# Kernel tuning notes

Hardware: AMD Instinct MI355X
Metric: run time of the kernel (lower is better)

## Reference

```python
import jax, jax.numpy as jnp
import numpy as np
from jax import lax

N, CIN, COUT, T, V = 32, 64, 128, 256, 25
IC = COUT // 4
EPS = 1e-5


def setup_inputs() -> dict:
    key = jax.random.key(0)
    ks = jax.random.split(key, 16)
    rn = lambda k, shape, s=0.05: jax.random.normal(k, shape, jnp.float32) * s
    inp = {
        'x': jax.random.normal(ks[0], (N, CIN, T, V), jnp.float32),
        'A': rn(ks[1], (V, V), 0.2),
        'w1': rn(ks[2], (IC, CIN)), 'b1': rn(ks[3], (IC,), 0.01),
        'w2': rn(ks[4], (IC, CIN)), 'b2': rn(ks[5], (IC,), 0.01),
        'w3': rn(ks[6], (COUT, CIN)), 'b3': rn(ks[7], (COUT,), 0.01),
        'w4': rn(ks[8], (COUT, CIN)), 'b4': rn(ks[9], (COUT,), 0.01),
        'bn1_g': jnp.ones((COUT,)), 'bn1_b': jnp.zeros((COUT,)),
        'bn1_m': rn(ks[10], (COUT,), 0.1), 'bn1_v': jnp.ones((COUT,)),
        'wt': rn(ks[11], (COUT, COUT, 9, 1)), 'bt': rn(ks[12], (COUT,), 0.01),
        'bn2_g': jnp.ones((COUT,)), 'bn2_b': jnp.zeros((COUT,)),
        'bn2_m': rn(ks[13], (COUT,), 0.1), 'bn2_v': jnp.ones((COUT,)),
        'wr': rn(ks[14], (COUT, CIN)), 'br': rn(ks[15], (COUT,), 0.01),
        'bnr_g': jnp.ones((COUT,)), 'bnr_b': jnp.zeros((COUT,)),
        'bnr_m': jnp.zeros((COUT,)), 'bnr_v': jnp.ones((COUT,)),
    }
    return inp


def _conv1x1(x, w, b):
    # 1x1 Conv2d over (T,V): pure channel mix. x: [N,C,T,V], w: [O,C]
    return jnp.einsum('oc,nctv->notv', w, x) + b[None, :, None, None]


def _bn(x, g, b, m, v):
    # BatchNorm2d in eval mode (running stats)
    scale = g / jnp.sqrt(v + EPS)
    return x * scale[None, :, None, None] + (b - m * scale)[None, :, None, None]


def _forward(x, A, w1, b1, w2, b2, w3, b3, w4, b4,
             bn1_g, bn1_b, bn1_m, bn1_v, wt, bt,
             bn2_g, bn2_b, bn2_m, bn2_v, wr, br,
             bnr_g, bnr_b, bnr_m, bnr_v):
    n, _, t, v = x.shape
    cout = w3.shape[0]
    ic = cout // 4
    x1 = _conv1x1(x, w1, b1).mean(axis=2)  # [N,IC,V]
    x2 = _conv1x1(x, w2, b2).mean(axis=2)  # [N,IC,V]
    a = jax.nn.softmax(x1[..., :, None] - x2[..., None, :], axis=-1)  # [N,IC,V,V]
    x3 = _conv1x1(x, w3, b3).reshape(n, 4, ic, t, v)
    y = jnp.einsum('ncuv,nmctv->nmctu', a, x3).reshape(n, cout, t, v)
    y = y + jnp.einsum('uv,nctv->nctu', A, _conv1x1(x, w4, b4))
    # tcn: BN -> ReLU -> Conv2d (9,1) pad (4,0) -> BN
    y = jax.nn.relu(_bn(y, bn1_g, bn1_b, bn1_m, bn1_v))
    y = lax.conv_general_dilated(
        y, wt, window_strides=(1, 1), padding=[(4, 4), (0, 0)],
        dimension_numbers=('NCHW', 'OIHW', 'NCHW')) + bt[None, :, None, None]
    y = _bn(y, bn2_g, bn2_b, bn2_m, bn2_v)
    # residual branch (in_channels != out_channels): 1x1 conv + BN
    res = _bn(_conv1x1(x, wr, br), bnr_g, bnr_b, bnr_m, bnr_v)
    return jax.nn.relu(y + res)


def reference(x, A, w1, b1, w2, b2, w3, b3, w4, b4,
              bn1_g, bn1_b, bn1_m, bn1_v, wt, bt,
              bn2_g, bn2_b, bn2_m, bn2_v, wr, br,
              bnr_g, bnr_b, bnr_m, bnr_v):
    return _forward(x, A, w1, b1, w2, b2, w3, b3, w4, b4,
                    bn1_g, bn1_b, bn1_m, bn1_v, wt, bt,
                    bn2_g, bn2_b, bn2_m, bn2_v, wr, br,
                    bnr_g, bnr_b, bnr_m, bnr_v)
```

## Files before the change

### kernel.cpp

```cpp
#include <hip/hip_runtime.h>
#include <hip/hip_bf16.h>

typedef unsigned short u16;
typedef unsigned int u32;
typedef unsigned long long u64;
typedef __attribute__((ext_vector_type(8))) short short8;
typedef __attribute__((ext_vector_type(4))) float f32x4;

#define DI __device__ __forceinline__

DI float b2f(u16 v){ u32 u = ((u32)v) << 16; float f; __builtin_memcpy(&f, &u, 4); return f; }
DI u16 f2bu(float f){ __hip_bfloat16 h = __float2bfloat16(f); u16 u; __builtin_memcpy(&u, &h, 2); return u; }

DI void gll16(const u16* g, u16* l){
  __builtin_amdgcn_global_load_lds((const __attribute__((address_space(1))) void*)g,
                                   (__attribute__((address_space(3))) void*)l, 16, 0, 0);
}

__global__ __launch_bounds__(256) void kprep(const float* __restrict__ x, u16* __restrict__ xT){
  __shared__ u16 tile[128*72];
  const int xb = blockIdx.x, n = blockIdx.y, tid = threadIdx.x;
  const int x0 = xb*128;
  const int ci = tid>>2, part = tid&3;
  const float* src = x + ((size_t)(n*64+ci))*6400 + x0 + part*32;
  #pragma unroll
  for (int i=0;i<8;i++){
    float4 f = ((const float4*)src)[i];
    const int col = part*32 + i*4;
    tile[(col+0)*72+ci] = f2bu(f.x);
    tile[(col+1)*72+ci] = f2bu(f.y);
    tile[(col+2)*72+ci] = f2bu(f.z);
    tile[(col+3)*72+ci] = f2bu(f.w);
  }
  __syncthreads();
  const int row = tid>>1, half = tid&1;
  short8* dst = (short8*)(xT + ((size_t)n*6400 + x0 + row)*64 + half*32);
  const short8* s8 = (const short8*)(tile + row*72 + half*32);
  #pragma unroll
  for (int i=0;i<4;i++) dst[i] = s8[i];
}

__global__ __launch_bounds__(256) void kzero(float* __restrict__ xm){
  const int i = blockIdx.x*1024 + threadIdx.x*4;
  float4 z = {0.f,0.f,0.f,0.f};
  *(float4*)(xm + i) = z;
}

__global__ __launch_bounds__(256) void kmean(const u16* __restrict__ xT, float* __restrict__ xm){
  __shared__ float part[4][1600];
  const int seg = blockIdx.x, n = blockIdx.y, tid = threadIdx.x;
  const int tg = tid>>6, c = tid&63;
  float acc[25];
  #pragma unroll
  for (int v=0;v<25;v++) acc[v]=0.f;
  for (int t = seg*32 + tg; t < seg*32 + 32; t += 4){
    const u16* base = xT + ((size_t)n*6400 + t*25)*64 + c;
    #pragma unroll
    for (int v=0;v<25;v++) acc[v] += b2f(base[v*64]);
  }
  #pragma unroll
  for (int v=0;v<25;v++) part[tg][v*64+c] = acc[v];
  __syncthreads();
  for (int idx = tid; idx < 1600; idx += 256){
    const int v = idx>>6, cc = idx&63;
    const float m = part[0][idx]+part[1][idx]+part[2][idx]+part[3][idx];
    atomicAdd(&xm[(n*64+cc)*25+v], m*(1.f/256.f));
  }
}

__global__ __launch_bounds__(64) void kp(const float* __restrict__ xm, const float* __restrict__ w2,
                                         const float* __restrict__ b2p, const float* __restrict__ Ab,
                                         float* __restrict__ p, float* __restrict__ rsA){
  const int c = blockIdx.x, n = blockIdx.y, lane = threadIdx.x;
  __shared__ float sc[32];
  __shared__ float red[2];
  float neg = 0.f;
  if (lane < 25){
    float acc = b2p[c];
    for (int k = 0; k < 64; k++) acc += w2[c*64 + k] * xm[(n*64 + k)*25 + lane];
    neg = -acc;
    sc[lane] = neg;
  }
  __syncthreads();
  if (lane == 0){
    float m = sc[0];
    for (int i = 1; i < 25; i++) m = fmaxf(m, sc[i]);
    red[0] = m;
  }
  __syncthreads();
  float e = 0.f;
  if (lane < 25){ e = expf(neg - red[0]); sc[lane] = e; }
  __syncthreads();
  if (lane == 0){
    float ssum = 0.f;
    for (int i = 0; i < 25; i++) ssum += sc[i];
    red[1] = ssum;
  }
  __syncthreads();
  if (lane < 25) p[(n*32 + c)*25 + lane] = e / red[1];
  if (n == 0 && c == 0 && lane < 25){
    float r = 0.f;
    for (int v = 0; v < 25; v++) r += Ab[lane*25 + v];
    rsA[lane] = r;
  }
}

__global__ __launch_bounds__(256) void kxa(const u16* __restrict__ xT, const float* __restrict__ Ab,
                                           u16* __restrict__ xA){
  __shared__ float xl[200*68];
  __shared__ float al[625];
  const int tc = blockIdx.x, n = blockIdx.y, tid = threadIdx.x;
  const int x0t = tc * 200;
  for (int i = tid; i < 625; i += 256) al[i] = Ab[i];
  for (int idx = tid; idx < 1600; idx += 256){
    const int r = idx>>3, i = idx&7;
    short8 v = *(const short8*)(xT + ((size_t)n*6400 + x0t + r)*64 + i*8);
    float* dst = xl + r*68 + i*8;
    #pragma unroll
    for (int e=0;e<8;e++) dst[e] = b2f((u16)v[e]);
  }
  __syncthreads();
  if (tid < 200){
    const int t_ = tid / 25, u = tid % 25;
    float acc[64];
    #pragma unroll
    for (int k = 0; k < 64; k++) acc[k] = 0.f;
    const float* arow = al + u*25;
    for (int v = 0; v < 25; v++){
      const float a = arow[v];
      const float* xr = xl + (t_*25 + v)*68;
      #pragma unroll
      for (int k = 0; k < 64; k++) acc[k] += a * xr[k];
    }
    u16* dst = xA + ((size_t)n*6400 + x0t + tid)*64;
    #pragma unroll
    for (int k = 0; k < 64; k += 4){
      u64 pk = (u64)f2bu(acc[k]) | ((u64)f2bu(acc[k+1])<<16)
             | ((u64)f2bu(acc[k+2])<<32) | ((u64)f2bu(acc[k+3])<<48);
      *(u64*)(dst + k) = pk;
    }
  }
}

__global__ __launch_bounds__(256) void kwt(const float* __restrict__ wt, u16* __restrict__ wtb){
  const int o = blockIdx.x*256 + threadIdx.x;
  const int dt = o >> 14, rem = o & 16383;
  wtb[o] = f2bu(wt[rem*9 + dt]);
}

__global__ __launch_bounds__(256) void kwr(const float* __restrict__ wrw, const float* __restrict__ g2,
                                           const float* __restrict__ v2, const float* __restrict__ gr,
                                           const float* __restrict__ vr, u16* __restrict__ wrb){
  const int o = blockIdx.x*256 + threadIdx.x;
  const int co = o >> 6;
  const float E0 = g2[co]*rsqrtf(v2[co]+1e-5f);
  const float R0 = gr[co]*rsqrtf(vr[co]+1e-5f);
  wrb[o] = f2bu(wrw[o]*R0/E0);
}

__global__ __launch_bounds__(256) void khpad(u16* __restrict__ h){
  const int n = blockIdx.x, side = blockIdx.y, tid = threadIdx.x;
  short8* base = (short8*)(h + ((size_t)n*6600 + (side ? 6500 : 0))*128);
  short8 z = {0,0,0,0,0,0,0,0};
  for (int i = tid; i < 1600; i += 256) base[i] = z;
}

__global__ __launch_bounds__(256) void ks(const u16* __restrict__ xT, const float* __restrict__ w3,
                                          const float* __restrict__ p, float* __restrict__ s){
  __shared__ __align__(16) char smem[53248];
  __shared__ float pL[800];
  u16* aL = (u16*)smem;
  u16* bL = (u16*)(smem + 18432);
  float* z3 = (float*)smem;
  const int xb = blockIdx.x, n = blockIdx.y, tid = threadIdx.x;
  const int x0 = xb*100, t0 = xb*4;
  const int row = tid >> 1, half = tid & 1;
  {
    const float* src = w3 + row*64 + half*32;
    u16* dst = aL + row*72 + half*32;
    #pragma unroll
    for (int i=0;i<8;i++){
      float4 f = ((const float4*)src)[i];
      dst[i*4+0]=f2bu(f.x); dst[i*4+1]=f2bu(f.y); dst[i*4+2]=f2bu(f.z); dst[i*4+3]=f2bu(f.w);
    }
  }
  {
    short8* dst = (short8*)(bL + row*72 + half*32);
    if (row < 100){
      const short8* src = (const short8*)(xT + ((size_t)n*6400 + x0 + row)*64 + half*32);
      #pragma unroll
      for (int i=0;i<4;i++) dst[i] = src[i];
    } else {
      short8 z = {0,0,0,0,0,0,0,0};
      #pragma unroll
      for (int i=0;i<4;i++) dst[i] = z;
    }
  }
  for (int i = tid; i < 800; i += 256) pL[i] = p[n*800 + i];
  __syncthreads();
  const int wave = tid>>6, lane = tid&63, q = lane>>4, l = lane&15;
  const int wr = wave>>1, wc = wave&1;
  f32x4 acc[4][4];
  #pragma unroll
  for (int i=0;i<4;i++)
    #pragma unroll
    for (int j=0;j<4;j++){ f32x4 z0 = {0.f,0.f,0.f,0.f}; acc[i][j] = z0; }
  #pragma unroll
  for (int ksi = 0; ksi < 2; ksi++){
    const int kb = ksi*32 + q*8;
    short8 af[4], bf[4];
    #pragma unroll
    for (int i=0;i<4;i++) af[i] = *(const short8*)(aL + (wr*64 + i*16 + l)*72 + kb);
    #pragma unroll
    for (int j=0;j<4;j++) bf[j] = *(const short8*)(bL + (wc*64 + j*16 + l)*72 + kb);
    #pragma unroll
    for (int i=0;i<4;i++)
      #pragma unroll
      for (int j=0;j<4;j++)
        acc[i][j] = __builtin_amdgcn_mfma_f32_16x16x32_bf16(af[i], bf[j], acc[i][j], 0, 0, 0);
  }
  __syncthreads();
  #pragma unroll
  for (int i=0;i<4;i++){
    const int co0 = wr*64 + i*16 + q*4;
    #pragma unroll
    for (int j=0;j<4;j++){
      const int colx = wc*64 + j*16 + l;
      if (colx < 100){
        #pragma unroll
        for (int r=0;r<4;r++) z3[(co0 + r)*104 + colx] = acc[i][j][r];
      }
    }
  }
  __syncthreads();
  for (int idx = tid; idx < 512; idx += 256){
    const int co = idx >> 2, tt = idx & 3;
    const float* zr = z3 + co*104 + tt*25;
    const float* pr = pL + (co & 31)*25;
    float acc2 = 0.f;
    #pragma unroll
    for (int v=0; v<25; v++) acc2 += zr[v]*pr[v];
    s[((size_t)n*128 + co)*256 + t0 + tt] = acc2;
  }
}

__global__ __launch_bounds__(256) void ky(const u16* __restrict__ xA, const float* __restrict__ w4,
      const float* __restrict__ s, const float* __restrict__ b3, const float* __restrict__ b4,
      const float* __restrict__ g1, const float* __restrict__ bb1, const float* __restrict__ m1,
      const float* __restrict__ v1, const float* __restrict__ rsA, u16* __restrict__ h){
  __shared__ __align__(16) u16 aL[128*72];
  __shared__ __align__(16) u16 bL[128*72];
  __shared__ float A0[128], A1[128], A2[128];
  __shared__ float sF[1024];
  __shared__ float rs[32];
  const int xb = blockIdx.x, n = blockIdx.y, tid = threadIdx.x;
  const int x0 = xb*128, tlo = x0/25;
  const int row = tid >> 1, half = tid & 1;
  {
    const float* src = w4 + row*64 + half*32;
    u16* dst = aL + row*72 + half*32;
    #pragma unroll
    for (int i=0;i<8;i++){
      float4 f = ((const float4*)src)[i];
      dst[i*4+0]=f2bu(f.x); dst[i*4+1]=f2bu(f.y); dst[i*4+2]=f2bu(f.z); dst[i*4+3]=f2bu(f.w);
    }
  }
  {
    const short8* src = (const short8*)(xA + ((size_t)n*6400 + x0 + row)*64 + half*32);
    short8* dst = (short8*)(bL + row*72 + half*32);
    #pragma unroll
    for (int i=0;i<4;i++) dst[i] = src[i];
  }
  if (tid < 128){
    const float scv = g1[tid] * rsqrtf(v1[tid] + 1e-5f);
    A0[tid] = scv;
    A1[tid] = scv * b4[tid];
    A2[tid] = bb1[tid] - m1[tid] * scv;
  }
  if (tid < 32) rs[tid] = (tid < 25) ? rsA[tid] : 0.f;
  __syncthreads();
  for (int idx = tid; idx < 1024; idx += 256){
    const int co = idx >> 3, tt = idx & 7;
    const int t = tlo + tt;
    const float sv = (t < 256) ? s[((size_t)n*128 + co)*256 + t] : 0.f;
    sF[idx] = A0[co] * (sv + b3[co]) + A2[co];
  }
  const int wave = tid>>6, lane = tid&63, q = lane>>4, l = lane&15;
  const int wr = wave>>1, wc = wave&1;
  f32x4 acc[4][4];
  #pragma unroll
  for (int i=0;i<4;i++)
    #pragma unroll
    for (int j=0;j<4;j++){ f32x4 z0 = {0.f,0.f,0.f,0.f}; acc[i][j] = z0; }
  #pragma unroll
  for (int ksi = 0; ksi < 2; ksi++){
    const int kb = ksi*32 + q*8;
    short8 af[4], bf[4];
    #pragma unroll
    for (int i=0;i<4;i++) af[i] = *(const short8*)(aL + (wr*64 + i*16 + l)*72 + kb);
    #pragma unroll
    for (int j=0;j<4;j++) bf[j] = *(const short8*)(bL + (wc*64 + j*16 + l)*72 + kb);
    #pragma unroll
    for (int i=0;i<4;i++)
      #pragma unroll
      for (int j=0;j<4;j++)
        acc[i][j] = __builtin_amdgcn_mfma_f32_16x16x32_bf16(af[i], bf[j], acc[i][j], 0, 0, 0);
  }
  __syncthreads();
  #pragma unroll
  for (int i=0;i<4;i++){
    const int co0 = wr*64 + i*16 + q*4;
    #pragma unroll
    for (int j=0;j<4;j++){
      const int colx = wc*64 + j*16 + l;
      const int xg = x0 + colx;
      const int u = xg % 25, tt = xg/25 - tlo;
      const float rsu = rs[u];
      u64 pk = 0;
      #pragma unroll
      for (int r=0;r<4;r++){
        const int co = co0 + r;
        float y = A0[co]*acc[i][j][r] + A1[co]*rsu + sF[co*8 + tt];
        y = fmaxf(y, 0.f);
        pk |= ((u64)f2bu(y)) << (16*r);
      }
      *(u64*)(h + ((size_t)n*6600 + xg + 100)*128 + co0) = pk;
    }
  }
}

__global__ __launch_bounds__(512, 2) void ktcn(const u16* __restrict__ h, const u16* __restrict__ wtb,
      const u16* __restrict__ wrb, const u16* __restrict__ xT,
      const float* __restrict__ bt, const float* __restrict__ g2, const float* __restrict__ bb2,
      const float* __restrict__ m2, const float* __restrict__ v2,
      const float* __restrict__ gr, const float* __restrict__ bbr, const float* __restrict__ mr,
      const float* __restrict__ vr, const float* __restrict__ brb,
      float* __restrict__ out){
  __shared__ __align__(16) char smem[149504];
  u16* hW = (u16*)smem;
  u16* Ab0 = (u16*)(smem + 83968);
  u16* Ab1 = (u16*)(smem + 116736);
  __shared__ float E0s[128], E1s[128];
  const int xb = blockIdx.x, n = blockIdx.y, tid = threadIdx.x;
  const int x0 = xb*128;
  const int wave = tid>>6, lane = tid&63, q = lane>>4, l = lane&15;
  const int wr2 = wave>>2, wc = wave&3;
  const u16* hbase = h + ((size_t)n*6600 + x0)*128;
  const u16* xtb = xT + ((size_t)n*6400 + x0)*64;

  #pragma unroll
  for (int it = 0; it < 10; ++it){
    const int ci = it*512 + tid;
    const int r = ci >> 4, c = ci & 15;
    gll16(hbase + r*128 + ((c ^ (r & 15))<<3), hW + ((it*512 + wave*64)<<3));
  }
  if (tid < 128){
    const int ci = 5120 + tid;
    const int r = ci >> 4, c = ci & 15;
    gll16(hbase + r*128 + ((c ^ (r & 15))<<3), hW + ((5120 + wave*64)<<3));
  }
  #pragma unroll
  for (int it = 0; it < 4; ++it){
    const int ci = it*512 + tid;
    const int r = ci >> 4, c = ci & 15;
    gll16(wtb + r*128 + ((c ^ (r & 15))<<3), Ab0 + ((it*512 + wave*64)<<3));
  }
  if (tid < 128){
    const float scv2 = g2[tid]*rsqrtf(v2[tid]+1e-5f);
    const float scvr = gr[tid]*rsqrtf(vr[tid]+1e-5f);
    E0s[tid] = scv2;
    E1s[tid] = scv2*bt[tid] + bb2[tid] - m2[tid]*scv2
             + (bbr[tid] - mr[tid]*scvr + scvr*brb[tid]);
  }
  f32x4 acc[4][2];
  #pragma unroll
  for (int i=0;i<4;i++)
    #pragma unroll
    for (int j=0;j<2;j++){ f32x4 z0 = {0.f,0.f,0.f,0.f}; acc[i][j] = z0; }
  __syncthreads();

  #pragma unroll 1
  for (int dt = 0; dt <= 9; ++dt){
    if (dt < 8){
      const u16* gA = wtb + (dt+1)*16384;
      u16* dA = (dt & 1) ? Ab0 : Ab1;
      #pragma unroll
      for (int it = 0; it < 4; ++it){
        const int ci = it*512 + tid;
        const int r = ci >> 4, c = ci & 15;
        gll16(gA + r*128 + ((c ^ (r & 15))<<3), dA + ((it*512 + wave*64)<<3));
      }
    } else if (dt == 8){
      #pragma unroll
      for (int it = 0; it < 2; ++it){
        const int ci = it*512 + tid;
        const int r = ci >> 3, c = ci & 7;
        gll16(wrb + r*64 + ((c ^ (r & 7))<<3), Ab1 + ((it*512 + wave*64)<<3));
      }
      #pragma unroll
      for (int it = 0; it < 2; ++it){
        const int ci = it*512 + tid;
        const int r = ci >> 3, c = ci & 7;
        gll16(xtb + r*64 + ((c ^ (r & 7))<<3), Ab1 + 8192 + ((it*512 + wave*64)<<3));
      }
    }
    if (dt < 9){
      const u16* A = (dt & 1) ? Ab1 : Ab0;
      #pragma unroll
      for (int ksi = 0; ksi < 4; ksi++){
        const int c0 = ksi*4 + q;
        short8 af[4], bf[2];
        #pragma unroll
        for (int i=0;i<4;i++){
          const int r = wr2*64 + i*16 + l;
          af[i] = *(const short8*)(A + (((r<<4) + (c0 ^ (r & 15)))<<3));
        }
        #pragma unroll
        for (int j=0;j<2;j++){
          const int r = dt*25 + wc*32 + j*16 + l;
          bf[j] = *(const short8*)(hW + (((r<<4) + (c0 ^ (r & 15)))<<3));
        }
        #pragma unroll
        for (int i=0;i<4;i++)
          #pragma unroll
          for (int j=0;j<2;j++)
            acc[i][j] = __builtin_amdgcn_mfma_f32_16x16x32_bf16(af[i], bf[j], acc[i][j], 0, 0, 0);
      }
    } else {
      const u16* A = Ab1;
      const u16* B = Ab1 + 8192;
      #pragma unroll
      for (int ksi = 0; ksi < 2; ksi++){
        const int c0 = ksi*4 + q;
        short8 af[4], bf[2];
        #pragma unroll
        for (int i=0;i<4;i++){
          const int r = wr2*64 + i*16 + l;
          af[i] = *(const short8*)(A + (((r<<3) + (c0 ^ (r & 7)))<<3));
        }
        #pragma unroll
        for (int j=0;j<2;j++){
          const int r = wc*32 + j*16 + l;
          bf[j] = *(const short8*)(B + (((r<<3) + (c0 ^ (r & 7)))<<3));
        }
        #pragma unroll
        for (int i=0;i<4;i++)
          #pragma unroll
          for (int j=0;j<2;j++)
            acc[i][j] = __builtin_amdgcn_mfma_f32_16x16x32_bf16(af[i], bf[j], acc[i][j], 0, 0, 0);
      }
    }
    __syncthreads();
  }

  #pragma unroll
  for (int i=0;i<4;i++){
    const int co0 = wr2*64 + i*16 + q*4;
    #pragma unroll
    for (int j=0;j<2;j++){
      const int colx = wc*32 + j*16 + l;
      #pragma unroll
      for (int r=0;r<4;r++){
        const float yv = E0s[co0+r]*acc[i][j][r] + E1s[co0+r];
        out[((size_t)n*128 + co0 + r)*6400 + x0 + colx] = fmaxf(yv, 0.f);
      }
    }
  }
}

extern "C" void kernel_launch(void* const* d_in, const int* in_sizes, int n_in,
                              void* d_out, int out_size, void* d_ws, size_t ws_size,
                              hipStream_t stream){
  const float* x   = (const float*)d_in[0];
  const float* Ab  = (const float*)d_in[1];
  const float* w2  = (const float*)d_in[4];
  const float* b2p = (const float*)d_in[5];
  const float* w3  = (const float*)d_in[6];
  const float* b3  = (const float*)d_in[7];
  const float* w4  = (const float*)d_in[8];
  const float* b4  = (const float*)d_in[9];
  const float* g1  = (const float*)d_in[10];
  const float* bb1 = (const float*)d_in[11];
  const float* m1  = (const float*)d_in[12];
  const float* v1  = (const float*)d_in[13];
  const float* wt  = (const float*)d_in[14];
  const float* bt  = (const float*)d_in[15];
  const float* g2  = (const float*)d_in[16];
  const float* bb2 = (const float*)d_in[17];
  const float* m2  = (const float*)d_in[18];
  const float* v2  = (const float*)d_in[19];
  const float* wrw = (const float*)d_in[20];
  const float* brb = (const float*)d_in[21];
  const float* gr  = (const float*)d_in[22];
  const float* bbr = (const float*)d_in[23];
  const float* mr  = (const float*)d_in[24];
  const float* vr  = (const float*)d_in[25];
  float* out = (float*)d_out;

  char* ws = (char*)d_ws;
  float* xm  = (float*)(ws);
  float* p   = (float*)(ws + 204800);
  float* rsA = (float*)(ws + 307200);
  float* s   = (float*)(ws + 307712);
  u16* xT    = (u16*)(ws + 4502016);
  u16* xA    = (u16*)(ws + 30716416);
  u16* h     = (u16*)(ws + 56930816);
  u16* wtb   = (u16*)(ws + 110998016);
  u16* wrb   = (u16*)(ws + 111292928);

  kprep<<<dim3(50,32), 256, 0, stream>>>(x, xT);
  kzero<<<50, 256, 0, stream>>>(xm);
  kmean<<<dim3(8,32), 256, 0, stream>>>(xT, xm);
  kp<<<dim3(32,32), 64, 0, stream>>>(xm, w2, b2p, Ab, p, rsA);
  kxa<<<dim3(32,32), 256, 0, stream>>>(xT, Ab, xA);
  kwt<<<576, 256, 0, stream>>>(wt, wtb);
  kwr<<<32, 256, 0, stream>>>(wrw, g2, v2, gr, vr, wrb);
  khpad<<<dim3(32,2), 256, 0, stream>>>(h);
  ks<<<dim3(64,32), 256, 0, stream>>>(xT, w3, p, s);
  ky<<<dim3(50,32), 256, 0, stream>>>(xA, w4, s, b3, b4, g1, bb1, m1, v1, rsA, h);
  ktcn<<<dim3(50,32), 512, 0, stream>>>(h, wtb, wrb, xT, bt, g2, bb2, m2, v2, gr, bbr, mr, vr, brb, out);
}
```

Before: 445.4 us.

## Fuse mean into prep, precast weights, and pipeline ktcn prologue loads

The separate kmean pass is folded into kprep, which sums each tile's columns from LDS and atomically adds the temporal mean, removing a re-read of xT. The w3 and w4 bf16 casts and the final BN scale and bias constants are computed once in an extended kwr kernel instead of in every block. ktcn now staggers its h-window loads across the first dt iterations and prefetches both weight buffers up front, using partial vmcnt waits instead of full barriers. The result is less prologue latency, at the cost of more fragile hand-managed wait counts.

```diff
diff --git a/kernel.cpp b/kernel.cpp
--- a/kernel.cpp
+++ b/kernel.cpp
@@ -17,7 +17,14 @@
                                    (__attribute__((address_space(3))) void*)l, 16, 0, 0);
 }
 
-__global__ __launch_bounds__(256) void kprep(const float* __restrict__ x, u16* __restrict__ xT){
+__global__ __launch_bounds__(256) void kzero(float* __restrict__ xm){
+  const int i = blockIdx.x*1024 + threadIdx.x*4;
+  float4 z = {0.f,0.f,0.f,0.f};
+  *(float4*)(xm + i) = z;
+}
+
+__global__ __launch_bounds__(256) void kprep(const float* __restrict__ x, u16* __restrict__ xT,
+                                             float* __restrict__ xm){
   __shared__ u16 tile[128*72];
   const int xb = blockIdx.x, n = blockIdx.y, tid = threadIdx.x;
   const int x0 = xb*128;
@@ -33,38 +40,20 @@
     tile[(col+3)*72+ci] = f2bu(f.w);
   }
   __syncthreads();
-  const int row = tid>>1, half = tid&1;
-  short8* dst = (short8*)(xT + ((size_t)n*6400 + x0 + row)*64 + half*32);
-  const short8* s8 = (const short8*)(tile + row*72 + half*32);
-  #pragma unroll
-  for (int i=0;i<4;i++) dst[i] = s8[i];
-}
-
-__global__ __launch_bounds__(256) void kzero(float* __restrict__ xm){
-  const int i = blockIdx.x*1024 + threadIdx.x*4;
-  float4 z = {0.f,0.f,0.f,0.f};
-  *(float4*)(xm + i) = z;
-}
-
-__global__ __launch_bounds__(256) void kmean(const u16* __restrict__ xT, float* __restrict__ xm){
-  __shared__ float part[4][1600];
-  const int seg = blockIdx.x, n = blockIdx.y, tid = threadIdx.x;
-  const int tg = tid>>6, c = tid&63;
-  float acc[25];
-  #pragma unroll
-  for (int v=0;v<25;v++) acc[v]=0.f;
-  for (int t = seg*32 + tg; t < seg*32 + 32; t += 4){
-    const u16* base = xT + ((size_t)n*6400 + t*25)*64 + c;
-    #pragma unroll
-    for (int v=0;v<25;v++) acc[v] += b2f(base[v*64]);
-  }
-  #pragma unroll
-  for (int v=0;v<25;v++) part[tg][v*64+c] = acc[v];
-  __syncthreads();
+  {
+    const int row = tid>>1, half = tid&1;
+    short8* dst = (short8*)(xT + ((size_t)n*6400 + x0 + row)*64 + half*32);
+    const short8* s8 = (const short8*)(tile + row*72 + half*32);
+    #pragma unroll
+    for (int i=0;i<4;i++) dst[i] = s8[i];
+  }
+  const int u0 = x0 % 25;
   for (int idx = tid; idx < 1600; idx += 256){
-    const int v = idx>>6, cc = idx&63;
-    const float m = part[0][idx]+part[1][idx]+part[2][idx]+part[3][idx];
-    atomicAdd(&xm[(n*64+cc)*25+v], m*(1.f/256.f));
+    const int v = idx >> 6, c2 = idx & 63;
+    int c0 = v - u0; if (c0 < 0) c0 += 25;
+    float sum = 0.f;
+    for (int c = c0; c < 128; c += 25) sum += b2f(tile[c*72 + c2]);
+    atomicAdd(&xm[(n*64 + c2)*25 + v], sum*(1.f/256.f));
   }
 }
 
@@ -149,13 +138,32 @@
 }
 
 __global__ __launch_bounds__(256) void kwr(const float* __restrict__ wrw, const float* __restrict__ g2,
-                                           const float* __restrict__ v2, const float* __restrict__ gr,
-                                           const float* __restrict__ vr, u16* __restrict__ wrb){
-  const int o = blockIdx.x*256 + threadIdx.x;
-  const int co = o >> 6;
-  const float E0 = g2[co]*rsqrtf(v2[co]+1e-5f);
-  const float R0 = gr[co]*rsqrtf(vr[co]+1e-5f);
-  wrb[o] = f2bu(wrw[o]*R0/E0);
+      const float* __restrict__ v2, const float* __restrict__ gr, const float* __restrict__ vr,
+      const float* __restrict__ w3, const float* __restrict__ w4,
+      const float* __restrict__ bt, const float* __restrict__ bb2, const float* __restrict__ m2,
+      const float* __restrict__ bbr, const float* __restrict__ mr, const float* __restrict__ brb,
+      u16* __restrict__ wrb, u16* __restrict__ w3b, u16* __restrict__ w4b,
+      float* __restrict__ e0, float* __restrict__ e1){
+  const int b = blockIdx.x, tid = threadIdx.x;
+  if (b < 32){
+    const int o = b*256 + tid;
+    const int co = o >> 6;
+    const float E0 = g2[co]*rsqrtf(v2[co]+1e-5f);
+    const float R0 = gr[co]*rsqrtf(vr[co]+1e-5f);
+    wrb[o] = f2bu(wrw[o]*R0/E0);
+  } else if (b < 64){
+    const int o = (b-32)*256 + tid;
+    w3b[o] = f2bu(w3[o]);
+  } else if (b < 96){
+    const int o = (b-64)*256 + tid;
+    w4b[o] = f2bu(w4[o]);
+  } else if (tid < 128){
+    const float scv2 = g2[tid]*rsqrtf(v2[tid]+1e-5f);
+    const float scvr = gr[tid]*rsqrtf(vr[tid]+1e-5f);
+    e0[tid] = scv2;
+    e1[tid] = scv2*bt[tid] + bb2[tid] - m2[tid]*scv2
+            + (bbr[tid] - mr[tid]*scvr + scvr*brb[tid]);
+  }
 }
 
 __global__ __launch_bounds__(256) void khpad(u16* __restrict__ h){
@@ -165,7 +173,7 @@
   for (int i = tid; i < 1600; i += 256) base[i] = z;
 }
 
-__global__ __launch_bounds__(256) void ks(const u16* __restrict__ xT, const float* __restrict__ w3,
+__global__ __launch_bounds__(256) void ks(const u16* __restrict__ xT, const u16* __restrict__ w3b,
                                           const float* __restrict__ p, float* __restrict__ s){
   __shared__ __align__(16) char smem[53248];
   __shared__ float pL[800];
@@ -176,13 +184,10 @@
   const int x0 = xb*100, t0 = xb*4;
   const int row = tid >> 1, half = tid & 1;
   {
-    const float* src = w3 + row*64 + half*32;
-    u16* dst = aL + row*72 + half*32;
-    #pragma unroll
-    for (int i=0;i<8;i++){
-      float4 f = ((const float4*)src)[i];
-      dst[i*4+0]=f2bu(f.x); dst[i*4+1]=f2bu(f.y); dst[i*4+2]=f2bu(f.z); dst[i*4+3]=f2bu(f.w);
-    }
+    short8* dst = (short8*)(aL + row*72 + half*32);
+    const short8* src = (const short8*)(w3b + row*64 + half*32);
+    #pragma unroll
+    for (int i=0;i<4;i++) dst[i] = src[i];
   }
   {
     short8* dst = (short8*)(bL + row*72 + half*32);
@@ -244,7 +249,7 @@
   }
 }
 
-__global__ __launch_bounds__(256) void ky(const u16* __restrict__ xA, const float* __restrict__ w4,
+__global__ __launch_bounds__(256) void ky(const u16* __restrict__ xA, const u16* __restrict__ w4b,
       const float* __restrict__ s, const float* __restrict__ b3, const float* __restrict__ b4,
       const float* __restrict__ g1, const float* __restrict__ bb1, const float* __restrict__ m1,
       const float* __restrict__ v1, const float* __restrict__ rsA, u16* __restrict__ h){
@@ -257,13 +262,10 @@
   const int x0 = xb*128, tlo = x0/25;
   const int row = tid >> 1, half = tid & 1;
   {
-    const float* src = w4 + row*64 + half*32;
-    u16* dst = aL + row*72 + half*32;
-    #pragma unroll
-    for (int i=0;i<8;i++){
-      float4 f = ((const float4*)src)[i];
-      dst[i*4+0]=f2bu(f.x); dst[i*4+1]=f2bu(f.y); dst[i*4+2]=f2bu(f.z); dst[i*4+3]=f2bu(f.w);
-    }
+    short8* dst = (short8*)(aL + row*72 + half*32);
+    const short8* src = (const short8*)(w4b + row*64 + half*32);
+    #pragma unroll
+    for (int i=0;i<4;i++) dst[i] = src[i];
   }
   {
     const short8* src = (const short8*)(xA + ((size_t)n*6400 + x0 + row)*64 + half*32);
@@ -331,16 +333,12 @@
 
 __global__ __launch_bounds__(512, 2) void ktcn(const u16* __restrict__ h, const u16* __restrict__ wtb,
       const u16* __restrict__ wrb, const u16* __restrict__ xT,
-      const float* __restrict__ bt, const float* __restrict__ g2, const float* __restrict__ bb2,
-      const float* __restrict__ m2, const float* __restrict__ v2,
-      const float* __restrict__ gr, const float* __restrict__ bbr, const float* __restrict__ mr,
-      const float* __restrict__ vr, const float* __restrict__ brb,
+      const float* __restrict__ e0g, const float* __restrict__ e1g,
       float* __restrict__ out){
   __shared__ __align__(16) char smem[149504];
   u16* hW = (u16*)smem;
   u16* Ab0 = (u16*)(smem + 83968);
   u16* Ab1 = (u16*)(smem + 116736);
-  __shared__ float E0s[128], E1s[128];
   const int xb = blockIdx.x, n = blockIdx.y, tid = threadIdx.x;
   const int x0 = xb*128;
   const int wave = tid>>6, lane = tid&63, q = lane>>4, l = lane&15;
@@ -348,16 +346,19 @@
   const u16* hbase = h + ((size_t)n*6600 + x0)*128;
   const u16* xtb = xT + ((size_t)n*6400 + x0)*64;
 
-  #pragma unroll
-  for (int it = 0; it < 10; ++it){
+  f32x4 e0r[4], e1r[4];
+  #pragma unroll
+  for (int i=0;i<4;i++){
+    const int co0 = wr2*64 + i*16 + q*4;
+    e0r[i] = *(const f32x4*)(e0g + co0);
+    e1r[i] = *(const f32x4*)(e1g + co0);
+  }
+
+  #pragma unroll
+  for (int it = 0; it < 4; ++it){
     const int ci = it*512 + tid;
     const int r = ci >> 4, c = ci & 15;
     gll16(hbase + r*128 + ((c ^ (r & 15))<<3), hW + ((it*512 + wave*64)<<3));
-  }
-  if (tid < 128){
-    const int ci = 5120 + tid;
-    const int r = ci >> 4, c = ci & 15;
-    gll16(hbase + r*128 + ((c ^ (r & 15))<<3), hW + ((5120 + wave*64)<<3));
   }
   #pragma unroll
   for (int it = 0; it < 4; ++it){
@@ -365,25 +366,34 @@
     const int r = ci >> 4, c = ci & 15;
     gll16(wtb + r*128 + ((c ^ (r & 15))<<3), Ab0 + ((it*512 + wave*64)<<3));
   }
-  if (tid < 128){
-    const float scv2 = g2[tid]*rsqrtf(v2[tid]+1e-5f);
-    const float scvr = gr[tid]*rsqrtf(vr[tid]+1e-5f);
-    E0s[tid] = scv2;
-    E1s[tid] = scv2*bt[tid] + bb2[tid] - m2[tid]*scv2
-             + (bbr[tid] - mr[tid]*scvr + scvr*brb[tid]);
-  }
+  #pragma unroll
+  for (int it = 0; it < 4; ++it){
+    const int ci = it*512 + tid;
+    const int r = ci >> 4, c = ci & 15;
+    gll16(wtb + 16384 + r*128 + ((c ^ (r & 15))<<3), Ab1 + ((it*512 + wave*64)<<3));
+  }
+  #pragma unroll
+  for (int it = 4; it < 6; ++it){
+    const int ci = it*512 + tid;
+    const int r = ci >> 4, c = ci & 15;
+    gll16(hbase + r*128 + ((c ^ (r & 15))<<3), hW + ((it*512 + wave*64)<<3));
+  }
+
   f32x4 acc[4][2];
   #pragma unroll
   for (int i=0;i<4;i++)
     #pragma unroll
     for (int j=0;j<2;j++){ f32x4 z0 = {0.f,0.f,0.f,0.f}; acc[i][j] = z0; }
-  __syncthreads();
+
+  asm volatile("s_waitcnt vmcnt(6) lgkmcnt(0)" ::: "memory");
+  __builtin_amdgcn_s_barrier();
+  __builtin_amdgcn_sched_barrier(0);
 
   #pragma unroll 1
   for (int dt = 0; dt <= 9; ++dt){
-    if (dt < 8){
+    if (dt >= 1 && dt <= 7){
       const u16* gA = wtb + (dt+1)*16384;
-      u16* dA = (dt & 1) ? Ab0 : Ab1;
+      u16* dA = ((dt+1) & 1) ? Ab1 : Ab0;
       #pragma unroll
       for (int it = 0; it < 4; ++it){
         const int ci = it*512 + tid;
@@ -404,6 +414,17 @@
         gll16(xtb + r*64 + ((c ^ (r & 7))<<3), Ab1 + 8192 + ((it*512 + wave*64)<<3));
       }
     }
+    if (dt >= 1 && dt <= 4){
+      const int it = 5 + dt;
+      const int ci = it*512 + tid;
+      const int r = ci >> 4, c = ci & 15;
+      gll16(hbase + r*128 + ((c ^ (r & 15))<<3), hW + ((it*512 + wave*64)<<3));
+      if (dt == 4 && tid < 128){
+        const int ci2 = 5120 + tid;
+        const int r2 = ci2 >> 4, c2 = ci2 & 15;
+        gll16(hbase + r2*128 + ((c2 ^ (r2 & 15))<<3), hW + ((5120 + wave*64)<<3));
+      }
+    }
     if (dt < 9){
       const u16* A = (dt & 1) ? Ab1 : Ab0;
       #pragma unroll
@@ -450,7 +471,15 @@
             acc[i][j] = __builtin_amdgcn_mfma_f32_16x16x32_bf16(af[i], bf[j], acc[i][j], 0, 0, 0);
       }
     }
-    __syncthreads();
+    if (dt < 9){
+      if (dt <= 4){
+        asm volatile("s_waitcnt vmcnt(1) lgkmcnt(0)" ::: "memory");
+        __builtin_amdgcn_s_barrier();
+        __builtin_amdgcn_sched_barrier(0);
+      } else {
+        __syncthreads();
+      }
+    }
   }
 
   #pragma unroll
@@ -461,7 +490,7 @@
       const int colx = wc*32 + j*16 + l;
       #pragma unroll
       for (int r=0;r<4;r++){
-        const float yv = E0s[co0+r]*acc[i][j][r] + E1s[co0+r];
+        const float yv = e0r[i][r]*acc[i][j][r] + e1r[i][r];
         out[((size_t)n*128 + co0 + r)*6400 + x0 + colx] = fmaxf(yv, 0.f);
       }
     }
@@ -507,16 +536,20 @@
   u16* h     = (u16*)(ws + 56930816);
   u16* wtb   = (u16*)(ws + 110998016);
   u16* wrb   = (u16*)(ws + 111292928);
-
-  kprep<<<dim3(50,32), 256, 0, stream>>>(x, xT);
+  u16* w3b   = (u16*)(ws + 111309312);
+  u16* w4b   = (u16*)(ws + 111325696);
+  float* e0  = (float*)(ws + 111342080);
+  float* e1  = (float*)(ws + 111342592);
+
   kzero<<<50, 256, 0, stream>>>(xm);
-  kmean<<<dim3(8,32), 256, 0, stream>>>(xT, xm);
+  kprep<<<dim3(50,32), 256, 0, stream>>>(x, xT, xm);
   kp<<<dim3(32,32), 64, 0, stream>>>(xm, w2, b2p, Ab, p, rsA);
   kxa<<<dim3(32,32), 256, 0, stream>>>(xT, Ab, xA);
   kwt<<<576, 256, 0, stream>>>(wt, wtb);
-  kwr<<<32, 256, 0, stream>>>(wrw, g2, v2, gr, vr, wrb);
+  kwr<<<97, 256, 0, stream>>>(wrw, g2, v2, gr, vr, w3, w4, bt, bb2, m2, bbr, mr, brb,
+                              wrb, w3b, w4b, e0, e1);
   khpad<<<dim3(32,2), 256, 0, stream>>>(h);
-  ks<<<dim3(64,32), 256, 0, stream>>>(xT, w3, p, s);
-  ky<<<dim3(50,32), 256, 0, stream>>>(xA, w4, s, b3, b4, g1, bb1, m1, v1, rsA, h);
-  ktcn<<<dim3(50,32), 512, 0, stream>>>(h, wtb, wrb, xT, bt, g2, bb2, m2, v2, gr, bbr, mr, vr, brb, out);
-}
+  ks<<<dim3(64,32), 256, 0, stream>>>(xT, w3b, p, s);
+  ky<<<dim3(50,32), 256, 0, stream>>>(xA, w4b, s, b3, b4, g1, bb1, m1, v1, rsA, h);
+  ktcn<<<dim3(50,32), 512, 0, stream>>>(h, wtb, wrb, xT, e0, e1, out);
+}
```

Result: slower. 507.3 us (+13.9%).
